# Kernel optimization log

Measured on AMD Instinct MI355X. Metric: run time of the kernel, lower is better.

The kernel has to match this reference:

```python
import jax, jax.numpy as jnp
import numpy as np

B, S, D = 4, 2048, 1024
H, DK, DV = 16, 64, 64


def setup_inputs() -> dict:
    key = jax.random.key(0)
    kx, kq, kk, kv, ko = jax.random.split(key, 5)
    scale = 0.02
    return {
        "x": jax.random.normal(kx, (B, S, D), dtype=jnp.float32),
        "Wq": jax.random.normal(kq, (H, D, DK), dtype=jnp.float32) * scale,
        "Wk": jax.random.normal(kk, (H, D, DK), dtype=jnp.float32) * scale,
        "Wv": jax.random.normal(kv, (H, D, DV), dtype=jnp.float32) * scale,
        "Wo": jax.random.normal(ko, (H * DV, D), dtype=jnp.float32) * scale,
    }


def reference(x, Wq, Wk, Wv, Wo):
    # Per-head projections, batched over heads with einsum (same math as
    # the original per-head Linear loop).
    q = jnp.einsum("bsd,hdk->bhsk", x, Wq)  # [B,H,S,DK]
    k = jnp.einsum("bsd,hdk->bhsk", x, Wk)  # [B,H,S,DK]
    v = jnp.einsum("bsd,hdv->bhsv", x, Wv)  # [B,H,S,DV]

    scores = jnp.einsum("bhqk,bhsk->bhqs", q, k) / jnp.sqrt(
        jnp.asarray(DK, dtype=x.dtype)
    )  # [B,H,S,S]
    # Causal mask: position q attends only to s <= q.
    causal = jnp.tril(jnp.ones((S, S), dtype=bool))
    scores = jnp.where(causal, scores, jnp.asarray(-1e9, dtype=scores.dtype))
    attn = jax.nn.softmax(scores, axis=-1)

    ctx = jnp.einsum("bhqs,bhsv->bhqv", attn, v)  # [B,H,S,DV]
    # Concat heads: [B,S,H*DV], then output projection (no bias).
    ctx = ctx.transpose(0, 2, 1, 3).reshape(B, S, H * DV)
    return ctx @ Wo  # [B,S,D]
```

## Files before the change

kernel.cpp:

```cpp
#include <hip/hip_runtime.h>
#include <hip/hip_bf16.h>

#define SB 2048
#define DM 1024
#define NH 16
#define HD 64
#define BB 4
#define MTOT (BB * SB)
#define NW (DM * DM)
#define QSCALE 0.1803368801111244f

typedef __attribute__((ext_vector_type(8))) short bf16x8;
typedef __attribute__((ext_vector_type(4))) short bf16x4;
typedef __attribute__((ext_vector_type(4))) float f32x4;
typedef __attribute__((ext_vector_type(4))) __fp16 f16x4;
typedef __attribute__((ext_vector_type(2))) __fp16 f16x2;

__device__ __forceinline__ short f2bf(float f) {
    union { float f; unsigned u; } a; a.f = f;
    unsigned r = (a.u + 0x7FFF + ((a.u >> 16) & 1)) >> 16;
    return (short)r;
}

__global__ __launch_bounds__(256) void cvt_all(const float* __restrict__ x,
                                               const float* __restrict__ Wq,
                                               const float* __restrict__ Wk,
                                               const float* __restrict__ Wv,
                                               const float* __restrict__ Wo,
                                               short* __restrict__ xb,
                                               short* __restrict__ wall,
                                               short* __restrict__ wot) {
    const int bid = blockIdx.x;
    const int t = threadIdx.x;
    if (bid < 4096) {
        const int i = (bid * 256 + t) * 8;
        float4 v0 = *(const float4*)(x + i);
        float4 v1 = *(const float4*)(x + i + 4);
        bf16x8 o = { f2bf(v0.x), f2bf(v0.y), f2bf(v0.z), f2bf(v0.w),
                     f2bf(v1.x), f2bf(v1.y), f2bf(v1.z), f2bf(v1.w) };
        *(bf16x8*)(xb + i) = o;
        return;
    }
    __shared__ float Ls[64][65];
    const int rem = bid - 4096;
    const int which = rem >> 8;
    const int rem2 = rem & 255;
    const float* in;
    short* out;
    int R, C;
    if (which < 3) {
        in = (which == 0) ? Wq : (which == 1) ? Wk : Wv;
        out = wall + (size_t)which * NW;
        R = DM; C = HD;
    } else {
        in = Wo; out = wot; R = DM; C = DM;
    }
    const int tilesC = C >> 6, tilesR = R >> 6;
    const int b = rem2 / (tilesR * tilesC);
    const int rr = rem2 % (tilesR * tilesC);
    const int R0 = (rr / tilesC) << 6;
    const int C0 = (rr % tilesC) << 6;
    const float* src = in + (size_t)b * R * C;
    short* dst = out + (size_t)b * R * C;
    const int r = t >> 2, c4 = (t & 3) << 4;
    const float* p = src + (size_t)(R0 + r) * C + C0 + c4;
#pragma unroll
    for (int u = 0; u < 16; u += 4) {
        float4 v = *(const float4*)(p + u);
        Ls[r][c4 + u] = v.x; Ls[r][c4 + u + 1] = v.y;
        Ls[r][c4 + u + 2] = v.z; Ls[r][c4 + u + 3] = v.w;
    }
    __syncthreads();
    const int cc = t >> 2, u2 = (t & 3) << 4;
    short* q = dst + (size_t)(C0 + cc) * R + R0 + u2;
    bf16x8 o0, o1;
#pragma unroll
    for (int j = 0; j < 8; ++j) o0[j] = f2bf(Ls[u2 + j][cc]);
#pragma unroll
    for (int j = 0; j < 8; ++j) o1[j] = f2bf(Ls[u2 + 8 + j][cc]);
    *(bf16x8*)(q) = o0;
    *(bf16x8*)(q + 8) = o1;
}

template <int MODE>
__global__ __launch_bounds__(256) void mm64(const short* __restrict__ A,
                                            const short* __restrict__ BT,
                                            short* __restrict__ qO,
                                            short* __restrict__ kO,
                                            _Float16* __restrict__ vO,
                                            float* __restrict__ fO) {
    __shared__ short sA[128 * 64];
    __shared__ short sB[128 * 64];
    const int t = threadIdx.x;
    const int lane = t & 63;
    const int w = t >> 6;
    const int wm = w >> 1, wn = w & 1;
    const int l15 = lane & 15, quad = lane >> 4;
    const int m0 = blockIdx.x * 128;
    const int n0 = blockIdx.y * 128;
    const bool isV = (MODE == 0) && (n0 >= 2048);

    f32x4 acc[4][4] = {};
    const int srow = t >> 3;
    const int schunk = t & 7;
    const int ssrc = ((schunk ^ (srow & 7)) << 3);
    const int sdst = (schunk << 3);
    const int r7 = l15 & 7;

    for (int k0 = 0; k0 < DM; k0 += 64) {
#pragma unroll
        for (int u = 0; u < 4; ++u) {
            const int row = u * 32 + srow;
            const short* ga = A + (size_t)(m0 + row) * DM + k0 + ssrc;
            const short* gb = BT + (size_t)(n0 + row) * DM + k0 + ssrc;
            __builtin_amdgcn_global_load_lds(
                (const __attribute__((address_space(1))) unsigned*)ga,
                (__attribute__((address_space(3))) unsigned*)&sA[(row << 6) + sdst],
                16, 0, 0);
            __builtin_amdgcn_global_load_lds(
                (const __attribute__((address_space(1))) unsigned*)gb,
                (__attribute__((address_space(3))) unsigned*)&sB[(row << 6) + sdst],
                16, 0, 0);
        }
        __syncthreads();

#pragma unroll
        for (int half = 0; half < 2; ++half) {
            bf16x8 af[4], bfr[4];
#pragma unroll
            for (int i = 0; i < 4; ++i) {
                const int ra = wm * 64 + i * 16 + l15;
                const int rb = wn * 64 + i * 16 + l15;
                const int ch = ((half * 4 + quad) ^ r7) << 3;
                af[i]  = *(const bf16x8*)&sA[(ra << 6) + ch];
                bfr[i] = *(const bf16x8*)&sB[(rb << 6) + ch];
            }
            if (isV) {
#pragma unroll
                for (int i = 0; i < 4; ++i)
#pragma unroll
                    for (int j = 0; j < 4; ++j)
                        acc[i][j] = __builtin_amdgcn_mfma_f32_16x16x32_bf16(af[i], bfr[j],
                                                                            acc[i][j], 0, 0, 0);
            } else {
#pragma unroll
                for (int i = 0; i < 4; ++i)
#pragma unroll
                    for (int j = 0; j < 4; ++j)
                        acc[i][j] = __builtin_amdgcn_mfma_f32_16x16x32_bf16(bfr[j], af[i],
                                                                            acc[i][j], 0, 0, 0);
            }
        }
        __syncthreads();
    }

    if (MODE == 1) {
#pragma unroll
        for (int i = 0; i < 4; ++i) {
            const int m = m0 + wm * 64 + i * 16 + l15;
#pragma unroll
            for (int j = 0; j < 4; ++j) {
                const int n = n0 + wn * 64 + j * 16 + quad * 4;
                f32x4 v = acc[i][j];
                *(float4*)&fO[(size_t)m * DM + n] = *(float4*)&v;
            }
        }
    } else if (isV) {
#pragma unroll
        for (int i = 0; i < 4; ++i) {
            const int m = m0 + wm * 64 + i * 16 + quad * 4;
            const int b = m >> 11, s0 = m & (SB - 1);
#pragma unroll
            for (int j = 0; j < 4; ++j) {
                const int nv = (n0 - 2048) + wn * 64 + j * 16 + l15;
                const int h = nv >> 6, d = nv & 63;
                f16x2 a = __builtin_amdgcn_cvt_pkrtz(acc[i][j][0], acc[i][j][1]);
                f16x2 b2 = __builtin_amdgcn_cvt_pkrtz(acc[i][j][2], acc[i][j][3]);
                f16x4 o = {a.x, a.y, b2.x, b2.y};
                *(f16x4*)&vO[((size_t)((b * NH + h) * HD + d)) * SB + s0] = o;
            }
        }
    } else {
#pragma unroll
        for (int i = 0; i < 4; ++i) {
            const int m = m0 + wm * 64 + i * 16 + l15;
            const int b = m >> 11, s = m & (SB - 1);
#pragma unroll
            for (int j = 0; j < 4; ++j) {
                const int n = n0 + wn * 64 + j * 16 + quad * 4;
                const int seg = n >> 10;
                const int h = (n & 1023) >> 6, d0 = n & 63;
                const float sc = (seg == 0) ? QSCALE : 1.0f;
                bf16x4 o;
#pragma unroll
                for (int r = 0; r < 4; ++r) o[r] = f2bf(acc[i][j][r] * sc);
                short* dst = (seg == 0) ? qO : kO;
                *(bf16x4*)&dst[(((size_t)(b * NH + h) * SB + s) << 6) + d0] = o;
            }
        }
    }
}

__global__ __launch_bounds__(256) void attn_mfma(const short* __restrict__ Q,
                                                 const short* __restrict__ K,
                                                 const _Float16* __restrict__ VT,
                                                 short* __restrict__ ctx) {
    __shared__ short    sK[2][64 * 64];
    __shared__ _Float16 sV[2][64 * 64];

    const int t = threadIdx.x;
    const int lane = t & 63, w = t >> 6;
    const int l15 = lane & 15, quad = lane >> 4;
    const int idx = blockIdx.x;
    const int bh = ((idx >> 7) << 3) | (idx & 7);
    const int pair = (idx >> 3) & 15;
    const int b = bh >> 4, h = bh & 15;
    const size_t hb = (size_t)bh * SB * HD;
    const short* Qb = Q + hb;
    const short* Kb = K + hb;
    const _Float16* Vb = VT + hb;

    const int srow = t >> 3;
    const int sch  = t & 7;
    const int srow2 = srow + 32;
    const int swl = l15 & 7;

    auto stage = [&](int k0, int bbuf) {
        __builtin_amdgcn_global_load_lds(
            (const __attribute__((address_space(1))) unsigned*)
                (Kb + (size_t)(k0 + srow) * HD + ((sch ^ (srow & 7)) << 3)),
            (__attribute__((address_space(3))) unsigned*)&sK[bbuf][t << 3], 16, 0, 0);
        __builtin_amdgcn_global_load_lds(
            (const __attribute__((address_space(1))) unsigned*)
                (Kb + (size_t)(k0 + srow2) * HD + ((sch ^ (srow2 & 7)) << 3)),
            (__attribute__((address_space(3))) unsigned*)&sK[bbuf][(t + 256) << 3], 16, 0, 0);
        __builtin_amdgcn_global_load_lds(
            (const __attribute__((address_space(1))) unsigned*)
                (Vb + (size_t)srow * SB + k0 + ((sch ^ (srow & 7)) << 3)),
            (__attribute__((address_space(3))) unsigned*)&sV[bbuf][t << 3], 16, 0, 0);
        __builtin_amdgcn_global_load_lds(
            (const __attribute__((address_space(1))) unsigned*)
                (Vb + (size_t)srow2 * SB + k0 + ((sch ^ (srow2 & 7)) << 3)),
            (__attribute__((address_space(3))) unsigned*)&sV[bbuf][(t + 256) << 3], 16, 0, 0);
    };

#pragma unroll
    for (int ph = 0; ph < 2; ++ph) {
        const int qt = ph ? (31 - pair) : pair;
        const int qw = qt * 64 + w * 16;

        bf16x8 aq[2];
#pragma unroll
        for (int hh = 0; hh < 2; ++hh)
            aq[hh] = *(const bf16x8*)(Qb + (size_t)(qw + l15) * HD + hh * 32 + quad * 8);

        f32x4 O[4] = {};
        float l_r = 0.f;

        __syncthreads();
        stage(0, 0);

#pragma unroll 2
        for (int kt = 0; kt <= qt; ++kt) {
            __syncthreads();
            if (kt < qt) stage((kt + 1) * 64, (kt + 1) & 1);

            const int buf = kt & 1;
            const bool diag = (kt == qt);
            const short* sKb = &sK[buf][0];
            const _Float16* sVb = &sV[buf][0];

            f32x4 sc[4] = {};
#pragma unroll
            for (int st = 0; st < 4; ++st) {
                const int row = st * 16 + l15;
#pragma unroll
                for (int hh = 0; hh < 2; ++hh) {
                    bf16x8 kf = *(const bf16x8*)&sKb[(row << 6) +
                                                     (((hh * 4 + quad) ^ swl) << 3)];
                    sc[st] = __builtin_amdgcn_mfma_f32_16x16x32_bf16(kf, aq[hh], sc[st], 0, 0, 0);
                }
            }

#pragma unroll
            for (int st = 0; st < 4; ++st) {
                if (diag && st > w) break;
                f16x4 vf[4];
                const int vch = ((st * 2 + (quad >> 1)) ^ swl) << 3;
#pragma unroll
                for (int dj = 0; dj < 4; ++dj)
                    vf[dj] = *(const f16x4*)&sVb[((dj * 16 + l15) << 6) + vch + (quad & 1) * 4];
                float p[4];
                if (!diag || st < w) {
#pragma unroll
                    for (int r = 0; r < 4; ++r) p[r] = __builtin_amdgcn_exp2f(sc[st][r]);
                } else {
#pragma unroll
                    for (int r = 0; r < 4; ++r)
                        p[r] = (quad * 4 + r <= l15) ? __builtin_amdgcn_exp2f(sc[st][r]) : 0.f;
                }
                l_r += (p[0] + p[1]) + (p[2] + p[3]);
                f16x2 pa = __builtin_amdgcn_cvt_pkrtz(p[0], p[1]);
                f16x2 pb = __builtin_amdgcn_cvt_pkrtz(p[2], p[3]);
                f16x4 pf = {pa.x, pa.y, pb.x, pb.y};
#pragma unroll
                for (int dj = 0; dj < 4; ++dj)
                    O[dj] = __builtin_amdgcn_mfma_f32_16x16x16f16(vf[dj], pf, O[dj], 0, 0, 0);
            }
        }

        float l = l_r;
        l += __shfl_xor(l, 16);
        l += __shfl_xor(l, 32);
        const float inv = 1.f / l;
        const int q = qw + l15;
#pragma unroll
        for (int dj = 0; dj < 4; ++dj) {
            bf16x4 o;
#pragma unroll
            for (int r = 0; r < 4; ++r) o[r] = f2bf(O[dj][r] * inv);
            *(bf16x4*)&ctx[(size_t)(b * SB + q) * DM + h * HD + dj * 16 + quad * 4] = o;
        }
    }
}

extern "C" void kernel_launch(void* const* d_in, const int* in_sizes, int n_in,
                              void* d_out, int out_size, void* d_ws, size_t ws_size,
                              hipStream_t stream) {
    const float* x  = (const float*)d_in[0];
    const float* Wq = (const float*)d_in[1];
    const float* Wk = (const float*)d_in[2];
    const float* Wv = (const float*)d_in[3];
    const float* Wo = (const float*)d_in[4];
    float* out = (float*)d_out;

    const size_t NX = (size_t)MTOT * DM;
    short* xb   = (short*)d_ws;
    short* wall = xb + NX;
    short* wot  = wall + 3 * (size_t)NW;
    short* qb   = wot + NW;
    short* kb   = qb + NX;
    short* vtb  = kb + NX;
    short* ctxb = vtb + NX;

    dim3 blk(256);
    cvt_all<<<4096 + 1024, blk, 0, stream>>>(x, Wq, Wk, Wv, Wo, xb, wall, wot);

    dim3 gqkv(MTOT / 128, 3072 / 128);
    mm64<0><<<gqkv, blk, 0, stream>>>(xb, wall, qb, kb, (_Float16*)vtb, nullptr);

    attn_mfma<<<dim3(1024), blk, 0, stream>>>(qb, kb, (const _Float16*)vtb, ctxb);

    dim3 gout(MTOT / 128, DM / 128);
    mm64<1><<<gout, blk, 0, stream>>>(ctxb, wot, nullptr, nullptr, nullptr, out);
}
```

Measured before the change: 239.8 us.

## Replace QKV projection GEMM with 256x256-tile, 8-wave pipelined kernel

Adds a new QKV projection kernel that computes 256x256 output tiles with 512 threads. Operands stream into four LDS buffers through direct global-to-LDS loads with a swizzled layout, and the blocks are remapped to improve L2 reuse. Loads are interleaved with MFMA phases using explicit waitcnt, barriers and setprio to overlap memory traffic with compute. It replaces the previous 128x128 mm64 launch. The larger tiles raise arithmetic intensity but leave only 384 blocks and add heavy register and LDS use (64 KB).

```diff
diff --git a/kernel.cpp b/kernel.cpp
--- a/kernel.cpp
+++ b/kernel.cpp
@@ -82,6 +82,210 @@
     *(bf16x8*)(q + 8) = o1;
 }
 
+__global__ __launch_bounds__(512, 2) void mmqkv(const short* __restrict__ A,
+                                                const short* __restrict__ BT,
+                                                short* __restrict__ qO,
+                                                short* __restrict__ kO,
+                                                _Float16* __restrict__ vO) {
+    __shared__ short sA[4][128 * 64];
+    __shared__ short sB[4][128 * 64];
+
+    const int t = threadIdx.x;
+    const int lane = t & 63, w = t >> 6;
+    const int l15 = lane & 15, quad = lane >> 4;
+    const int wq_r = w >> 2, wq_c = w & 3;
+    const int r7 = l15 & 7;
+
+    int id = blockIdx.x;
+    id = (id & 7) * 48 + (id >> 3);
+    const int m0 = (id / 12) * 256;
+    const int n0 = (id % 12) * 256;
+    const bool isV = (n0 >= 2048);
+
+    const short* Ah0 = A + (size_t)m0 * DM;
+    const short* Ah1 = Ah0 + (size_t)128 * DM;
+    const short* Bh0 = BT + (size_t)n0 * DM;
+    const short* Bh1 = Bh0 + (size_t)128 * DM;
+
+    auto STG = [&](short* lds, const short* g) {
+#pragma unroll
+        for (int u = 0; u < 2; ++u) {
+            const int idx = (w << 1) | u;
+            const int row = (idx << 3) + (lane >> 3);
+            __builtin_amdgcn_global_load_lds(
+                (const __attribute__((address_space(1))) unsigned*)
+                    (g + (size_t)row * DM + (((lane & 7) ^ (lane >> 3)) << 3)),
+                (__attribute__((address_space(3))) unsigned*)
+                    (lds + (((idx << 6) + lane) << 3)),
+                16, 0, 0);
+        }
+    };
+    auto LDA = [&](bf16x8 (&af)[4][2], const short* slot) {
+#pragma unroll
+        for (int i = 0; i < 4; ++i) {
+            const int row = wq_r * 64 + i * 16 + l15;
+#pragma unroll
+            for (int kh = 0; kh < 2; ++kh)
+                af[i][kh] = *(const bf16x8*)&slot[(row << 6) +
+                                                  ((((kh << 2) | quad) ^ r7) << 3)];
+        }
+    };
+    auto LDB = [&](bf16x8 (&bf)[2][2], const short* slot) {
+#pragma unroll
+        for (int j = 0; j < 2; ++j) {
+            const int row = wq_c * 32 + j * 16 + l15;
+#pragma unroll
+            for (int kh = 0; kh < 2; ++kh)
+                bf[j][kh] = *(const bf16x8*)&slot[(row << 6) +
+                                                  ((((kh << 2) | quad) ^ r7) << 3)];
+        }
+    };
+
+    f32x4 acc[2][2][4][2] = {};
+
+    auto FMAC = [&](f32x4 (&ac)[4][2], bf16x8 (&af)[4][2], bf16x8 (&bf)[2][2]) {
+        __builtin_amdgcn_s_setprio(1);
+        if (isV) {
+#pragma unroll
+            for (int i = 0; i < 4; ++i)
+#pragma unroll
+                for (int j = 0; j < 2; ++j)
+#pragma unroll
+                    for (int kh = 0; kh < 2; ++kh)
+                        ac[i][j] = __builtin_amdgcn_mfma_f32_16x16x32_bf16(
+                            af[i][kh], bf[j][kh], ac[i][j], 0, 0, 0);
+        } else {
+#pragma unroll
+            for (int i = 0; i < 4; ++i)
+#pragma unroll
+                for (int j = 0; j < 2; ++j)
+#pragma unroll
+                    for (int kh = 0; kh < 2; ++kh)
+                        ac[i][j] = __builtin_amdgcn_mfma_f32_16x16x32_bf16(
+                            bf[j][kh], af[i][kh], ac[i][j], 0, 0, 0);
+        }
+        __builtin_amdgcn_s_setprio(0);
+    };
+
+#define BARR __builtin_amdgcn_s_barrier()
+#define LGKM0 asm volatile("s_waitcnt lgkmcnt(0)" ::: "memory")
+#define VMC6 asm volatile("s_waitcnt vmcnt(6)" ::: "memory")
+#define VMC0 asm volatile("s_waitcnt vmcnt(0)" ::: "memory")
+
+    STG(sA[0], Ah0);
+    STG(sB[0], Bh0);
+    STG(sB[1], Bh1);
+    STG(sA[1], Ah1);
+    STG(sA[2], Ah0 + 64);
+    STG(sB[2], Bh0 + 64);
+    STG(sB[3], Bh1 + 64);
+    VMC6;
+    BARR;
+
+#pragma unroll 1
+    for (int it = 0; it < 8; ++it) {
+        const int k0 = it << 7;
+        const bool nl = (it < 7);
+        bf16x8 aF[4][2], bF0[2][2], bF1[2][2];
+
+        LDA(aF, sA[0]); LDB(bF0, sB[0]);
+        STG(sA[3], Ah1 + k0 + 64);
+        BARR; LGKM0;
+        FMAC(acc[0][0], aF, bF0);
+        BARR;
+
+        LDB(bF1, sB[1]);
+        if (nl) STG(sA[0], Ah0 + k0 + 128);
+        BARR; LGKM0;
+        FMAC(acc[0][1], aF, bF1);
+        BARR;
+
+        LDA(aF, sA[1]);
+        if (nl) STG(sB[0], Bh0 + k0 + 128);
+        BARR; LGKM0;
+        FMAC(acc[1][0], aF, bF0);
+        BARR;
+
+        if (nl) STG(sB[1], Bh1 + k0 + 128);
+        FMAC(acc[1][1], aF, bF1);
+        if (nl) { VMC6; } else { VMC0; }
+        BARR;
+
+        LDA(aF, sA[2]); LDB(bF0, sB[2]);
+        if (nl) STG(sA[1], Ah1 + k0 + 128);
+        BARR; LGKM0;
+        FMAC(acc[0][0], aF, bF0);
+        BARR;
+
+        LDB(bF1, sB[3]);
+        if (nl) STG(sA[2], Ah0 + k0 + 192);
+        BARR; LGKM0;
+        FMAC(acc[0][1], aF, bF1);
+        BARR;
+
+        LDA(aF, sA[3]);
+        if (nl) STG(sB[2], Bh0 + k0 + 192);
+        BARR; LGKM0;
+        FMAC(acc[1][0], aF, bF0);
+        BARR;
+
+        if (nl) STG(sB[3], Bh1 + k0 + 192);
+        FMAC(acc[1][1], aF, bF1);
+        if (nl) VMC6;
+        BARR;
+    }
+
+#undef BARR
+#undef LGKM0
+#undef VMC6
+#undef VMC0
+
+    if (!isV) {
+#pragma unroll
+        for (int qa = 0; qa < 2; ++qa)
+#pragma unroll
+        for (int qb = 0; qb < 2; ++qb)
+#pragma unroll
+        for (int i = 0; i < 4; ++i) {
+            const int m = m0 + qa * 128 + wq_r * 64 + i * 16 + l15;
+            const int b = m >> 11, s = m & (SB - 1);
+#pragma unroll
+            for (int j = 0; j < 2; ++j) {
+                const int n = n0 + qb * 128 + wq_c * 32 + j * 16 + quad * 4;
+                const int seg = n >> 10;
+                const int h = (n & 1023) >> 6, d0 = n & 63;
+                const float sc = (seg == 0) ? QSCALE : 1.0f;
+                bf16x4 o;
+#pragma unroll
+                for (int r = 0; r < 4; ++r) o[r] = f2bf(acc[qa][qb][i][j][r] * sc);
+                short* dst = (seg == 0) ? qO : kO;
+                *(bf16x4*)&dst[(((size_t)(b * NH + h) * SB + s) << 6) + d0] = o;
+            }
+        }
+    } else {
+#pragma unroll
+        for (int qa = 0; qa < 2; ++qa)
+#pragma unroll
+        for (int qb = 0; qb < 2; ++qb)
+#pragma unroll
+        for (int i = 0; i < 4; ++i) {
+            const int m = m0 + qa * 128 + wq_r * 64 + i * 16 + quad * 4;
+            const int b = m >> 11, s0 = m & (SB - 1);
+#pragma unroll
+            for (int j = 0; j < 2; ++j) {
+                const int nv = (n0 - 2048) + qb * 128 + wq_c * 32 + j * 16 + l15;
+                const int h = nv >> 6, d = nv & 63;
+                f16x2 a = __builtin_amdgcn_cvt_pkrtz(acc[qa][qb][i][j][0],
+                                                     acc[qa][qb][i][j][1]);
+                f16x2 b2 = __builtin_amdgcn_cvt_pkrtz(acc[qa][qb][i][j][2],
+                                                      acc[qa][qb][i][j][3]);
+                f16x4 o = {a.x, a.y, b2.x, b2.y};
+                *(f16x4*)&vO[((size_t)((b * NH + h) * HD + d)) * SB + s0] = o;
+            }
+        }
+    }
+}
+
 template <int MODE>
 __global__ __launch_bounds__(256) void mm64(const short* __restrict__ A,
                                             const short* __restrict__ BT,
@@ -346,8 +550,7 @@
     dim3 blk(256);
     cvt_all<<<4096 + 1024, blk, 0, stream>>>(x, Wq, Wk, Wv, Wo, xb, wall, wot);
 
-    dim3 gqkv(MTOT / 128, 3072 / 128);
-    mm64<0><<<gqkv, blk, 0, stream>>>(xb, wall, qb, kb, (_Float16*)vtb, nullptr);
+    mmqkv<<<dim3(384), dim3(512), 0, stream>>>(xb, wall, qb, kb, (_Float16*)vtb);
 
     attn_mfma<<<dim3(1024), blk, 0, stream>>>(qb, kb, (const _Float16*)vtb, ctxb);
 
```

Result: slower. 313.5 us (+30.7%).
